# Kernel optimization log

Measured on AMD Instinct MI355X. Metric: run time of the kernel, lower is better.

The kernel has to match this reference:

```python
import jax, jax.numpy as jnp
import numpy as np

B, T, C, NH = 32, 512, 1024, 16
DH = C // NH


def _rope_tables(seq_len, dim):
    # matches RotaryEmbedding: inv_freq over even indices; emb=cat(freqs,freqs),
    # but only the first dim//2 columns (== freqs) are ever sliced out.
    inv = 1.0 / (10000.0 ** (np.arange(0, dim, 2, dtype=np.float32) / dim))
    freqs = np.arange(seq_len, dtype=np.float32)[:, None] * inv[None, :]  # [T, dh/2]
    return jnp.asarray(np.cos(freqs)), jnp.asarray(np.sin(freqs))


def _apply_rope(x, cos, sin):
    # x: [B,T,H,D] with D even; interleaved-pair rotation as in the torch code
    b, t, h, d = x.shape
    d2 = d // 2
    xv = x.reshape(b, t, h, d2, 2)
    x0, x1 = xv[..., 0], xv[..., 1]
    c = cos[None, :t, None, :]  # [1,T,1,d2]
    s = sin[None, :t, None, :]
    o0 = x0 * c - x1 * s
    o1 = x0 * s + x1 * c
    return jnp.stack([o0, o1], axis=-1).reshape(b, t, h, d)


def setup_inputs() -> dict:
    key = jax.random.key(0)
    ks = jax.random.split(key, 5)
    scale = 0.02
    return {
        "x": jax.random.normal(ks[0], (B, T, C), dtype=jnp.float32),
        "Wq": jax.random.normal(ks[1], (C, C), dtype=jnp.float32) * scale,
        "Wk": jax.random.normal(ks[2], (C, C), dtype=jnp.float32) * scale,
        "Wv": jax.random.normal(ks[3], (C, C), dtype=jnp.float32) * scale,
        "Wo": jax.random.normal(ks[4], (C, C), dtype=jnp.float32) * scale,
    }


def reference(x, Wq, Wk, Wv, Wo):
    b, t, c = x.shape
    cos, sin = _rope_tables(t, DH)
    # torch nn.Linear(bias=False): y = x @ W.T
    q = (x @ Wq.T).reshape(b, t, NH, DH)
    k = (x @ Wk.T).reshape(b, t, NH, DH)
    v = (x @ Wv.T).reshape(b, t, NH, DH)
    q = _apply_rope(q, cos, sin)
    k = _apply_rope(k, cos, sin)
    # [B,H,T,D]
    q = q.transpose(0, 2, 1, 3)
    k = k.transpose(0, 2, 1, 3)
    v = v.transpose(0, 2, 1, 3)
    # fp32 scores + fp32 softmax (explicit, matches the torch upcast)
    att = jnp.einsum("bhqd,bhkd->bhqk", q.astype(jnp.float32), k.astype(jnp.float32))
    att = att * (DH ** -0.5)
    att = jax.nn.softmax(att, axis=-1).astype(v.dtype)
    # dropout omitted (eval mode)
    out = jnp.einsum("bhqk,bhkd->bhqd", att, v)
    out = out.transpose(0, 2, 1, 3).reshape(b, t, c)
    return out @ Wo.T
```

## Files before the change

kernel.cpp:

```cpp
#include <hip/hip_runtime.h>
#include <hip/hip_bf16.h>
#include <stdint.h>

#define B_  32
#define T_  512
#define C_  1024
#define NH_ 16
#define DH_ 64
#define NT_ 32

typedef __attribute__((ext_vector_type(8))) __bf16 bf16x8;
typedef __attribute__((ext_vector_type(4))) __bf16 bf16x4;
typedef __attribute__((ext_vector_type(4))) float  f32x4;

__device__ __forceinline__ void gload_lds16(const void* g, void* lds) {
  __builtin_amdgcn_global_load_lds(
      (const __attribute__((address_space(1))) void*)(uintptr_t)g,
      (__attribute__((address_space(3))) void*)(uint32_t)(uintptr_t)lds,
      16, 0, 0);
}

__global__ void prep_kernel(const float* __restrict__ x,
                            const float* __restrict__ Wq, const float* __restrict__ Wk,
                            const float* __restrict__ Wv, const float* __restrict__ Wo,
                            __bf16* __restrict__ xb, __bf16* __restrict__ wqkv,
                            __bf16* __restrict__ wob,
                            float* __restrict__ cosT, float* __restrict__ sinT) {
  int i = blockIdx.x * blockDim.x + threadIdx.x;
  if (i < 4194304) {
    f32x4 v = *(const f32x4*)(x + (size_t)i * 4);
    bf16x4 o;
    o[0] = (__bf16)v[0]; o[1] = (__bf16)v[1]; o[2] = (__bf16)v[2]; o[3] = (__bf16)v[3];
    *(bf16x4*)(xb + (size_t)i * 4) = o;
  } else if (i < 5242880) {
    int j = i - 4194304;
    int w = j >> 18, idx = j & 262143;
    const float* src = (w == 0) ? Wq : (w == 1) ? Wk : (w == 2) ? Wv : Wo;
    __bf16* dst = (w == 3) ? wob : wqkv + (size_t)w * 1048576;
    f32x4 v = *(const f32x4*)(src + (size_t)idx * 4);
    bf16x4 o;
    o[0] = (__bf16)v[0]; o[1] = (__bf16)v[1]; o[2] = (__bf16)v[2]; o[3] = (__bf16)v[3];
    *(bf16x4*)(dst + (size_t)idx * 4) = o;
  } else if (i < 5259264) {
    int j = i - 5242880;
    int t = j >> 5, f = j & 31;
    float inv = powf(10000.0f, -(float)(2 * f) / 64.0f);
    float fr = (float)t * inv;
    cosT[j] = cosf(fr);
    sinT[j] = sinf(fr);
  }
}

template <int MODE>
__global__ __launch_bounds__(512, 2) void gemm8(
    const __bf16* __restrict__ A,
    const __bf16* __restrict__ W0, const __bf16* __restrict__ W1, const __bf16* __restrict__ W2,
    __bf16* __restrict__ q, __bf16* __restrict__ k, __bf16* __restrict__ vt,
    float* __restrict__ outp) {
  extern __shared__ __bf16 lds[];
  __bf16* As = lds;
  __bf16* Bs = lds + 32768;
  const int K = C_;
  int tid = threadIdx.x;
  int lane = tid & 63, wave = tid >> 6;
  int ql = lane & 15, g = lane >> 4;
  int wr = wave >> 2, wc = wave & 3;

  constexpr int BNH = (MODE == 0) ? 6 : 2;
  int bid = blockIdx.x;
  int xcd = bid & 7, local = bid >> 3;
  int bm = (xcd >> 1) * 16 + local / BNH;
  int bn = (xcd & 1) * BNH + local % BNH;

  const __bf16* Ag = A + (size_t)bm * 256 * K;
  const __bf16* Wg;
  if (MODE == 0) {
    int mat = bn >> 2;
    const __bf16* Wsel = (mat == 0) ? W0 : (mat == 1) ? W1 : W2;
    Wg = Wsel + (size_t)(bn & 3) * 256 * K;
  } else {
    Wg = W0 + (size_t)bn * 256 * K;
  }

  int off0 = tid * 8;
  int off1 = off0 + 4096;
  int ar0 = off0 >> 5, ac0 = (off0 & 31) ^ (((ar0 >> 1) & 3) << 3);
  int ar1 = off1 >> 5, ac1 = (off1 & 31) ^ (((ar1 >> 1) & 3) << 3);
  size_t as0 = (size_t)ar0 * K + ac0;
  size_t as1 = (size_t)ar1 * K + ac1;

  int colsw = (g * 8) ^ (((ql >> 1) & 3) << 3);
  int aoff[8], boff[4];
#pragma unroll
  for (int m = 0; m < 8; m++) aoff[m] = (wr * 128 + m * 16 + ql) * 32 + colsw;
#pragma unroll
  for (int n = 0; n < 4; n++) boff[n] = (wc * 64 + n * 16 + ql) * 32 + colsw;

#define STAGE_(kt)                                   \
  {                                                  \
    int bq_ = ((kt) & 3) * 8192;                     \
    const __bf16* asrc_ = Ag + (kt) * 32;            \
    const __bf16* bsrc_ = Wg + (kt) * 32;            \
    gload_lds16(asrc_ + as0, As + bq_ + off0);       \
    gload_lds16(asrc_ + as1, As + bq_ + off1);       \
    gload_lds16(bsrc_ + as0, Bs + bq_ + off0);       \
    gload_lds16(bsrc_ + as1, Bs + bq_ + off1);       \
  }

  STAGE_(0); STAGE_(1); STAGE_(2);
  asm volatile("s_waitcnt vmcnt(8)" ::: "memory");
  __builtin_amdgcn_s_barrier();
  __builtin_amdgcn_sched_barrier(0);

  f32x4 acc[8][4] = {};
  for (int t = 0; t < NT_; ++t) {
    if (t + 3 < NT_) STAGE_(t + 3);
    int bq = (t & 3) * 8192;
    bf16x8 af[8], bfr[4];
#pragma unroll
    for (int m = 0; m < 8; m++) af[m] = *(const bf16x8*)(As + bq + aoff[m]);
#pragma unroll
    for (int n = 0; n < 4; n++) bfr[n] = *(const bf16x8*)(Bs + bq + boff[n]);
    __builtin_amdgcn_s_setprio(1);
#pragma unroll
    for (int m = 0; m < 8; m++)
#pragma unroll
      for (int n = 0; n < 4; n++)
        acc[m][n] = __builtin_amdgcn_mfma_f32_16x16x32_bf16(af[m], bfr[n], acc[m][n], 0, 0, 0);
    __builtin_amdgcn_s_setprio(0);
    if (t < NT_ - 3)       { asm volatile("s_waitcnt vmcnt(8)" ::: "memory"); }
    else if (t == NT_ - 3) { asm volatile("s_waitcnt vmcnt(4)" ::: "memory"); }
    else                   { asm volatile("s_waitcnt vmcnt(0)" ::: "memory"); }
    __builtin_amdgcn_s_barrier();
    __builtin_amdgcn_sched_barrier(0);
  }
#undef STAGE_

  int r0 = bm * 256 + wr * 128;
  int c0 = bn * 256 + wc * 64;
  if (MODE == 0) {
    int mat = c0 >> 10;
#pragma unroll
    for (int m = 0; m < 8; m++) {
      int row = r0 + m * 16 + g * 4;
      int b = row >> 9, tt = row & 511;
#pragma unroll
      for (int n = 0; n < 4; n++) {
        int col = c0 + n * 16 + ql;
        int h = (col & 1023) >> 6, d = col & 63;
        if (mat == 2) {
          bf16x4 ov;
#pragma unroll
          for (int r = 0; r < 4; r++) ov[r] = (__bf16)acc[m][n][r];
          *(bf16x4*)(vt + ((size_t)(b * NH_ + h) * DH_ + d) * T_ + tt) = ov;
        } else {
          __bf16* dst = (mat == 0 ? q : k) + ((size_t)(b * NH_ + h) * T_ + tt) * DH_ + d;
#pragma unroll
          for (int r = 0; r < 4; r++) dst[r * DH_] = (__bf16)acc[m][n][r];
        }
      }
    }
  } else {
#pragma unroll
    for (int m = 0; m < 8; m++) {
      int row = r0 + m * 16 + g * 4;
#pragma unroll
      for (int r = 0; r < 4; r++)
#pragma unroll
        for (int n = 0; n < 4; n++)
          outp[(size_t)(row + r) * C_ + c0 + n * 16 + ql] = acc[m][n][r];
    }
  }
}

__global__ __launch_bounds__(512, 2) void attn_kernel(
    const __bf16* __restrict__ qg, const __bf16* __restrict__ kg,
    const __bf16* __restrict__ vg, __bf16* __restrict__ ao,
    const float* __restrict__ cosT, const float* __restrict__ sinT) {
  extern __shared__ char smem[];
  __bf16* Klds = (__bf16*)smem;
  __bf16* Vlds = (__bf16*)(smem + 65536);

  int tid = threadIdx.x;
  int lane = tid & 63, wave = tid >> 6;
  int ql = lane & 15, g = lane >> 4;
  int bh = blockIdx.x;
  int b = bh >> 4, h = bh & 15;
  const __bf16* qp = qg + (size_t)bh * (T_ * DH_);
  const __bf16* kp = kg + (size_t)bh * (T_ * DH_);
  const __bf16* vp = vg + (size_t)bh * (T_ * DH_);

  {
    int cb = tid & 7;
    int rb = tid >> 3;
#pragma unroll
    for (int i = 0; i < 8; i++) {
      int row = rb + i * 64;
      bf16x8 raw = *(const bf16x8*)(kp + (size_t)row * DH_ + cb * 8);
      f32x4 c4 = *(const f32x4*)(cosT + row * 32 + cb * 4);
      f32x4 s4 = *(const f32x4*)(sinT + row * 32 + cb * 4);
      bf16x8 out;
#pragma unroll
      for (int p = 0; p < 4; p++) {
        float a0 = (float)raw[2 * p], a1 = (float)raw[2 * p + 1];
        out[2 * p]     = (__bf16)(a0 * c4[p] - a1 * s4[p]);
        out[2 * p + 1] = (__bf16)(a0 * s4[p] + a1 * c4[p]);
      }
      *(bf16x8*)(Klds + row * 64 + ((cb ^ (row & 7)) * 8)) = out;
    }
  }
  {
    int d = tid >> 3;
    int cb = tid & 7;
    const __bf16* vrow = vp + (size_t)d * T_;
#pragma unroll
    for (int i = 0; i < 8; i++) {
      int c8 = cb + i * 8;
      bf16x8 raw = *(const bf16x8*)(vrow + c8 * 8);
      *(bf16x8*)(Vlds + d * 516 + c8 * 8) = raw;
    }
  }

  int q0 = wave * 64;
  bf16x8 qf[4][2];
#pragma unroll
  for (int s = 0; s < 4; s++)
#pragma unroll
    for (int kk = 0; kk < 2; kk++) {
      int tq = q0 + s * 16 + ql;
      bf16x8 raw = *(const bf16x8*)(qp + (size_t)tq * DH_ + kk * 32 + g * 8);
      int fb = tq * 32 + kk * 16 + g * 4;
      f32x4 c4 = *(const f32x4*)(cosT + fb);
      f32x4 s4 = *(const f32x4*)(sinT + fb);
      bf16x8 out;
#pragma unroll
      for (int p = 0; p < 4; p++) {
        float a0 = (float)raw[2 * p], a1 = (float)raw[2 * p + 1];
        out[2 * p]     = (__bf16)(0.125f * (a0 * c4[p] - a1 * s4[p]));
        out[2 * p + 1] = (__bf16)(0.125f * (a0 * s4[p] + a1 * c4[p]));
      }
      qf[s][kk] = out;
    }

  __syncthreads();

  f32x4 o[4][4] = {};
  float mrow[4] = {-1e30f, -1e30f, -1e30f, -1e30f};
  float lrow[4] = {0.f, 0.f, 0.f, 0.f};

  for (int kv0 = 0; kv0 < T_; kv0 += 32) {
    bf16x8 kf[2][2], vf[4];
#pragma unroll
    for (int sub = 0; sub < 2; sub++)
#pragma unroll
      for (int kk = 0; kk < 2; kk++) {
        int t = kv0 + sub * 16 + ql;
        int cc = kk * 4 + g;
        kf[sub][kk] = *(const bf16x8*)(Klds + t * 64 + ((cc ^ (t & 7)) * 8));
      }
#pragma unroll
    for (int c = 0; c < 4; c++) {
      int d = c * 16 + ql;
      bf16x4 vlo = *(const bf16x4*)(Vlds + d * 516 + kv0 + g * 4);
      bf16x4 vhi = *(const bf16x4*)(Vlds + d * 516 + kv0 + 16 + g * 4);
#pragma unroll
      for (int r = 0; r < 4; r++) { vf[c][r] = vlo[r]; vf[c][4 + r] = vhi[r]; }
    }

#pragma unroll
    for (int s = 0; s < 4; s++) {
      f32x4 s0 = {0.f, 0.f, 0.f, 0.f}, s1 = {0.f, 0.f, 0.f, 0.f};
      __builtin_amdgcn_s_setprio(1);
#pragma unroll
      for (int kk = 0; kk < 2; kk++) {
        s0 = __builtin_amdgcn_mfma_f32_16x16x32_bf16(kf[0][kk], qf[s][kk], s0, 0, 0, 0);
        s1 = __builtin_amdgcn_mfma_f32_16x16x32_bf16(kf[1][kk], qf[s][kk], s1, 0, 0, 0);
      }
      __builtin_amdgcn_s_setprio(0);
      float tm = s0[0];
#pragma unroll
      for (int r = 1; r < 4; r++) tm = fmaxf(tm, s0[r]);
#pragma unroll
      for (int r = 0; r < 4; r++) tm = fmaxf(tm, s1[r]);
      tm = fmaxf(tm, __shfl_xor(tm, 16));
      tm = fmaxf(tm, __shfl_xor(tm, 32));
      if (!__all(tm <= mrow[s] + 8.0f)) {
        float mnew = fmaxf(mrow[s], tm);
        float corr = __expf(mrow[s] - mnew);
        mrow[s] = mnew;
        lrow[s] *= corr;
#pragma unroll
        for (int c = 0; c < 4; c++) o[s][c] *= corr;
      }
      float p0[4], p1[4], ps = 0.f;
#pragma unroll
      for (int r = 0; r < 4; r++) {
        p0[r] = __expf(s0[r] - mrow[s]);
        p1[r] = __expf(s1[r] - mrow[s]);
        ps += p0[r] + p1[r];
      }
      ps += __shfl_xor(ps, 16);
      ps += __shfl_xor(ps, 32);
      lrow[s] += ps;
      bf16x8 pb;
#pragma unroll
      for (int r = 0; r < 4; r++) {
        pb[r]     = (__bf16)p0[r];
        pb[4 + r] = (__bf16)p1[r];
      }
      __builtin_amdgcn_s_setprio(1);
#pragma unroll
      for (int c = 0; c < 4; c++)
        o[s][c] = __builtin_amdgcn_mfma_f32_16x16x32_bf16(vf[c], pb, o[s][c], 0, 0, 0);
      __builtin_amdgcn_s_setprio(0);
    }
  }

#pragma unroll
  for (int s = 0; s < 4; s++) {
    float inv = 1.0f / lrow[s];
    size_t row = (size_t)b * T_ + q0 + s * 16 + ql;
    size_t baseo = row * C_ + h * DH_;
#pragma unroll
    for (int c = 0; c < 4; c++) {
      bf16x4 ov;
#pragma unroll
      for (int r = 0; r < 4; r++) ov[r] = (__bf16)(o[s][c][r] * inv);
      *(bf16x4*)(ao + baseo + c * 16 + g * 4) = ov;
    }
  }
}

extern "C" void kernel_launch(void* const* d_in, const int* in_sizes, int n_in,
                              void* d_out, int out_size, void* d_ws, size_t ws_size,
                              hipStream_t stream) {
  (void)in_sizes; (void)n_in; (void)out_size; (void)ws_size;
  const float* x  = (const float*)d_in[0];
  const float* Wq = (const float*)d_in[1];
  const float* Wk = (const float*)d_in[2];
  const float* Wv = (const float*)d_in[3];
  const float* Wo = (const float*)d_in[4];

  char* ws = (char*)d_ws;
  char* od = (char*)d_out;
  float* outp = (float*)d_out;

  __bf16* qb = (__bf16*)(od);
  __bf16* kb = (__bf16*)(od + 33554432);
  __bf16* xb   = (__bf16*)(ws);
  __bf16* vtb  = (__bf16*)(ws + 33554432);
  __bf16* wqkv = (__bf16*)(ws + 67108864);
  __bf16* wob  = (__bf16*)(ws + 73400320);
  float*  cosT = (float*)(ws + 75497472);
  float*  sinT = (float*)(ws + 75563008);
  __bf16* aob  = xb;

  auto k0 = gemm8<0>; auto k1 = gemm8<1>;
  hipFuncSetAttribute((const void*)k0, hipFuncAttributeMaxDynamicSharedMemorySize, 131072);
  hipFuncSetAttribute((const void*)k1, hipFuncAttributeMaxDynamicSharedMemorySize, 131072);
  hipFuncSetAttribute((const void*)attn_kernel, hipFuncAttributeMaxDynamicSharedMemorySize, 131584);

  prep_kernel<<<dim3(20544), dim3(256), 0, stream>>>(
      x, Wq, Wk, Wv, Wo, xb, wqkv, wob, cosT, sinT);

  gemm8<0><<<dim3(768), dim3(512), 131072, stream>>>(
      xb, wqkv, wqkv + 1048576, wqkv + 2097152, qb, kb, vtb, nullptr);

  attn_kernel<<<dim3(B_ * NH_), dim3(512), 131584, stream>>>(
      qb, kb, vtb, aob, cosT, sinT);

  gemm8<1><<<dim3(256), dim3(512), 131072, stream>>>(
      aob, wob, nullptr, nullptr, nullptr, nullptr, nullptr, outp);
}
```

Baseline: 258.3 us.

## Split GEMM main loop into two half-phases interleaving A/B staging with MFMA

The GEMM k-loop is split into two phases, each doing half of the M fragments. A-tile global-to-LDS loads are issued in the first phase and B-tile loads in the second. Extra barriers and lgkmcnt waits stagger the LDS reads, global loads and MFMA work across waves, in the style of a ping-pong schedule. The aim is better overlap of memory traffic with matrix math, at the cost of four barriers per iteration instead of one.

```diff
diff --git a/kernel.cpp b/kernel.cpp
--- a/kernel.cpp
+++ b/kernel.cpp
@@ -96,45 +96,68 @@
 #pragma unroll
   for (int n = 0; n < 4; n++) boff[n] = (wc * 64 + n * 16 + ql) * 32 + colsw;
 
-#define STAGE_(kt)                                   \
+#define STAGE_A_(kt)                                 \
   {                                                  \
     int bq_ = ((kt) & 3) * 8192;                     \
     const __bf16* asrc_ = Ag + (kt) * 32;            \
-    const __bf16* bsrc_ = Wg + (kt) * 32;            \
     gload_lds16(asrc_ + as0, As + bq_ + off0);       \
     gload_lds16(asrc_ + as1, As + bq_ + off1);       \
+  }
+#define STAGE_B_(kt)                                 \
+  {                                                  \
+    int bq_ = ((kt) & 3) * 8192;                     \
+    const __bf16* bsrc_ = Wg + (kt) * 32;            \
     gload_lds16(bsrc_ + as0, Bs + bq_ + off0);       \
     gload_lds16(bsrc_ + as1, Bs + bq_ + off1);       \
   }
 
-  STAGE_(0); STAGE_(1); STAGE_(2);
+  STAGE_A_(0); STAGE_B_(0);
+  STAGE_A_(1); STAGE_B_(1);
+  STAGE_A_(2); STAGE_B_(2);
   asm volatile("s_waitcnt vmcnt(8)" ::: "memory");
   __builtin_amdgcn_s_barrier();
   __builtin_amdgcn_sched_barrier(0);
 
   f32x4 acc[8][4] = {};
   for (int t = 0; t < NT_; ++t) {
-    if (t + 3 < NT_) STAGE_(t + 3);
     int bq = (t & 3) * 8192;
-    bf16x8 af[8], bfr[4];
-#pragma unroll
-    for (int m = 0; m < 8; m++) af[m] = *(const bf16x8*)(As + bq + aoff[m]);
+    bf16x8 af[4], af2[4], bfr[4];
+#pragma unroll
+    for (int m = 0; m < 4; m++) af[m] = *(const bf16x8*)(As + bq + aoff[m]);
 #pragma unroll
     for (int n = 0; n < 4; n++) bfr[n] = *(const bf16x8*)(Bs + bq + boff[n]);
+    if (t + 3 < NT_) STAGE_A_(t + 3);
+    __builtin_amdgcn_s_barrier();
+    asm volatile("s_waitcnt lgkmcnt(0)" ::: "memory");
+    __builtin_amdgcn_sched_barrier(0);
     __builtin_amdgcn_s_setprio(1);
 #pragma unroll
-    for (int m = 0; m < 8; m++)
+    for (int m = 0; m < 4; m++)
 #pragma unroll
       for (int n = 0; n < 4; n++)
         acc[m][n] = __builtin_amdgcn_mfma_f32_16x16x32_bf16(af[m], bfr[n], acc[m][n], 0, 0, 0);
     __builtin_amdgcn_s_setprio(0);
+    __builtin_amdgcn_s_barrier();
+#pragma unroll
+    for (int m = 0; m < 4; m++) af2[m] = *(const bf16x8*)(As + bq + aoff[4 + m]);
+    if (t + 3 < NT_) STAGE_B_(t + 3);
     if (t < NT_ - 3)       { asm volatile("s_waitcnt vmcnt(8)" ::: "memory"); }
     else if (t == NT_ - 3) { asm volatile("s_waitcnt vmcnt(4)" ::: "memory"); }
     else                   { asm volatile("s_waitcnt vmcnt(0)" ::: "memory"); }
     __builtin_amdgcn_s_barrier();
+    asm volatile("s_waitcnt lgkmcnt(0)" ::: "memory");
     __builtin_amdgcn_sched_barrier(0);
-  }
-#undef STAGE_
+    __builtin_amdgcn_s_setprio(1);
+#pragma unroll
+    for (int m = 0; m < 4; m++)
+#pragma unroll
+      for (int n = 0; n < 4; n++)
+        acc[4 + m][n] = __builtin_amdgcn_mfma_f32_16x16x32_bf16(af2[m], bfr[n], acc[4 + m][n], 0, 0, 0);
+    __builtin_amdgcn_s_setprio(0);
+    __builtin_amdgcn_s_barrier();
+  }
+#undef STAGE_A_
+#undef STAGE_B_
 
   int r0 = bm * 256 + wr * 128;
   int c0 = bn * 256 + wc * 64;
```

Measured after the change: 258.4 us. No clear change (+0.0%).

## Restructure GEMM main loop into eight-phase ping-pong schedule with interleaved loads

Applied to the files above, without the earlier changes.

Replaces the four-slot, one-tile-per-iteration GEMM pipeline with a two-buffer scheme that uses 64-wide K tiles split into half-tiles. Each tile is processed in eight phases. Each phase loads half the A fragments (and B every other phase), issues one global-to-LDS stage, and runs 16 MFMAs between barriers. The aim is finer interleaving of LDS reads, global prefetch and MFMA work, hiding latency better than the previous coarse per-tile schedule. The cost is many more barriers per K-step and more complex vmcnt bookkeeping, which could stall waves or introduce hazards if the counts are off.

```diff
diff --git a/kernel.cpp b/kernel.cpp
--- a/kernel.cpp
+++ b/kernel.cpp
@@ -7,7 +7,6 @@
 #define C_  1024
 #define NH_ 16
 #define DH_ 64
-#define NT_ 32
 
 typedef __attribute__((ext_vector_type(8))) __bf16 bf16x8;
 typedef __attribute__((ext_vector_type(4))) __bf16 bf16x4;
@@ -58,9 +57,8 @@
     __bf16* __restrict__ q, __bf16* __restrict__ k, __bf16* __restrict__ vt,
     float* __restrict__ outp) {
   extern __shared__ __bf16 lds[];
-  __bf16* As = lds;
-  __bf16* Bs = lds + 32768;
   const int K = C_;
+  const int NH8 = 64;
   int tid = threadIdx.x;
   int lane = tid & 63, wave = tid >> 6;
   int ql = lane & 15, g = lane >> 4;
@@ -82,59 +80,81 @@
     Wg = W0 + (size_t)bn * 256 * K;
   }
 
-  int off0 = tid * 8;
-  int off1 = off0 + 4096;
-  int ar0 = off0 >> 5, ac0 = (off0 & 31) ^ (((ar0 >> 1) & 3) << 3);
-  int ar1 = off1 >> 5, ac1 = (off1 & 31) ^ (((ar1 >> 1) & 3) << 3);
-  size_t as0 = (size_t)ar0 * K + ac0;
-  size_t as1 = (size_t)ar1 * K + ac1;
-
-  int colsw = (g * 8) ^ (((ql >> 1) & 3) << 3);
-  int aoff[8], boff[4];
-#pragma unroll
-  for (int m = 0; m < 8; m++) aoff[m] = (wr * 128 + m * 16 + ql) * 32 + colsw;
-#pragma unroll
-  for (int n = 0; n < 4; n++) boff[n] = (wc * 64 + n * 16 + ql) * 32 + colsw;
-
-#define STAGE_(kt)                                   \
-  {                                                  \
-    int bq_ = ((kt) & 3) * 8192;                     \
-    const __bf16* asrc_ = Ag + (kt) * 32;            \
-    const __bf16* bsrc_ = Wg + (kt) * 32;            \
-    gload_lds16(asrc_ + as0, As + bq_ + off0);       \
-    gload_lds16(asrc_ + as1, As + bq_ + off1);       \
-    gload_lds16(bsrc_ + as0, Bs + bq_ + off0);       \
-    gload_lds16(bsrc_ + as1, Bs + bq_ + off1);       \
-  }
-
-  STAGE_(0); STAGE_(1); STAGE_(2);
-  asm volatile("s_waitcnt vmcnt(8)" ::: "memory");
+  int schunk = (tid & 3) ^ ((tid >> 3) & 3);
+  size_t stg_base = (size_t)(tid >> 2) * K + schunk * 8;
+
+  int xsw = (g ^ ((ql >> 1) & 3)) * 8;
+  int aoffW[8], boffW[4];
+#pragma unroll
+  for (int m = 0; m < 8; m++) aoffW[m] = (wr * 128 + m * 16 + ql) * 32 + xsw;
+#pragma unroll
+  for (int n = 0; n < 4; n++) boffW[n] = (wc * 64 + n * 16 + ql) * 32 + xsw;
+
+#define STAGE_H(h)                                                          \
+  if ((h) < NH8) {                                                          \
+    int tl_ = (h) >> 2, pt_ = (h) & 3;                                      \
+    const __bf16* s_ = ((pt_ & 1) ? Wg : Ag) + stg_base +                   \
+                       (size_t)tl_ * 64 + (pt_ >> 1) * 32;                  \
+    __bf16* d_ = lds + (((tl_ & 1) * 4 + pt_) * 8192) + tid * 8;            \
+    gload_lds16(s_, d_);                                                    \
+    gload_lds16(s_ + (size_t)128 * K, d_ + 4096);                           \
+  }
+
+#define PH(TP, KK, MLO, RB, SH, VM)                                         \
+  {                                                                         \
+    const __bf16* abase_ = lds + (((TP) * 4 + ((KK) ? 2 : 0)) * 8192);      \
+    _Pragma("unroll")                                                       \
+    for (int mm = 0; mm < 4; mm++)                                          \
+      a[mm] = *(const bf16x8*)(abase_ + aoffW[(MLO) + mm]);                 \
+    if (RB) {                                                               \
+      const __bf16* bbase_ = lds + (((TP) * 4 + ((KK) ? 3 : 1)) * 8192);    \
+      _Pragma("unroll")                                                     \
+      for (int n = 0; n < 4; n++)                                           \
+        b[n] = *(const bf16x8*)(bbase_ + boffW[n]);                         \
+    }                                                                       \
+    STAGE_H(SH);                                                            \
+    __builtin_amdgcn_s_barrier();                                           \
+    asm volatile("s_waitcnt lgkmcnt(0)" ::: "memory");                      \
+    __builtin_amdgcn_sched_barrier(0);                                      \
+    __builtin_amdgcn_s_setprio(1);                                          \
+    _Pragma("unroll")                                                       \
+    for (int mm = 0; mm < 4; mm++)                                          \
+      _Pragma("unroll")                                                     \
+      for (int n = 0; n < 4; n++)                                           \
+        acc[(MLO) + mm][n] = __builtin_amdgcn_mfma_f32_16x16x32_bf16(       \
+            a[mm], b[n], acc[(MLO) + mm][n], 0, 0, 0);                      \
+    __builtin_amdgcn_s_setprio(0);                                          \
+    {                                                                       \
+      int vm_ = (VM);                                                       \
+      if (vm_ == 0)      { asm volatile("s_waitcnt vmcnt(0)" ::: "memory"); } \
+      else if (vm_ > 0)  { asm volatile("s_waitcnt vmcnt(6)" ::: "memory"); } \
+    }                                                                       \
+    __builtin_amdgcn_s_barrier();                                           \
+  }
+
+  STAGE_H(0); STAGE_H(1); STAGE_H(2); STAGE_H(3);
+  STAGE_H(4); STAGE_H(5); STAGE_H(6);
+  asm volatile("s_waitcnt vmcnt(6)" ::: "memory");
   __builtin_amdgcn_s_barrier();
   __builtin_amdgcn_sched_barrier(0);
 
   f32x4 acc[8][4] = {};
-  for (int t = 0; t < NT_; ++t) {
-    if (t + 3 < NT_) STAGE_(t + 3);
-    int bq = (t & 3) * 8192;
-    bf16x8 af[8], bfr[4];
-#pragma unroll
-    for (int m = 0; m < 8; m++) af[m] = *(const bf16x8*)(As + bq + aoff[m]);
-#pragma unroll
-    for (int n = 0; n < 4; n++) bfr[n] = *(const bf16x8*)(Bs + bq + boff[n]);
-    __builtin_amdgcn_s_setprio(1);
-#pragma unroll
-    for (int m = 0; m < 8; m++)
-#pragma unroll
-      for (int n = 0; n < 4; n++)
-        acc[m][n] = __builtin_amdgcn_mfma_f32_16x16x32_bf16(af[m], bfr[n], acc[m][n], 0, 0, 0);
-    __builtin_amdgcn_s_setprio(0);
-    if (t < NT_ - 3)       { asm volatile("s_waitcnt vmcnt(8)" ::: "memory"); }
-    else if (t == NT_ - 3) { asm volatile("s_waitcnt vmcnt(4)" ::: "memory"); }
-    else                   { asm volatile("s_waitcnt vmcnt(0)" ::: "memory"); }
-    __builtin_amdgcn_s_barrier();
-    __builtin_amdgcn_sched_barrier(0);
-  }
-#undef STAGE_
+  bf16x8 a[4], b[4];
+  for (int i = 0; i < 8; ++i) {
+    int hb = 8 * i;
+    int vm4 = (i == 7) ? 0 : 6;
+    int vm8 = (i == 7) ? -1 : 6;
+    PH(0, 0, 0, 1, hb + 7,  -1)
+    PH(0, 0, 4, 0, hb + 8,  -1)
+    PH(0, 1, 0, 1, hb + 9,  -1)
+    PH(0, 1, 4, 0, hb + 10, vm4)
+    PH(1, 0, 0, 1, hb + 11, -1)
+    PH(1, 0, 4, 0, hb + 12, -1)
+    PH(1, 1, 0, 1, hb + 13, -1)
+    PH(1, 1, 4, 0, hb + 14, vm8)
+  }
+#undef PH
+#undef STAGE_H
 
   int r0 = bm * 256 + wr * 128;
   int c0 = bn * 256 + wc * 64;
@@ -143,7 +163,7 @@
 #pragma unroll
     for (int m = 0; m < 8; m++) {
       int row = r0 + m * 16 + g * 4;
-      int b = row >> 9, tt = row & 511;
+      int bb = row >> 9, tt = row & 511;
 #pragma unroll
       for (int n = 0; n < 4; n++) {
         int col = c0 + n * 16 + ql;
@@ -152,9 +172,9 @@
           bf16x4 ov;
 #pragma unroll
           for (int r = 0; r < 4; r++) ov[r] = (__bf16)acc[m][n][r];
-          *(bf16x4*)(vt + ((size_t)(b * NH_ + h) * DH_ + d) * T_ + tt) = ov;
+          *(bf16x4*)(vt + ((size_t)(bb * NH_ + h) * DH_ + d) * T_ + tt) = ov;
         } else {
-          __bf16* dst = (mat == 0 ? q : k) + ((size_t)(b * NH_ + h) * T_ + tt) * DH_ + d;
+          __bf16* dst = (mat == 0 ? q : k) + ((size_t)(bb * NH_ + h) * T_ + tt) * DH_ + d;
 #pragma unroll
           for (int r = 0; r < 4; r++) dst[r * DH_] = (__bf16)acc[m][n][r];
         }
```

Result: no change. 254.8 us (-1.4%).
